# Kernel optimization log

Hardware: AMD Instinct MI355X
Metric: run time of the kernel (lower is better)

Reference implementation:

```python
import jax, jax.numpy as jnp
import numpy as np

EPS = 1e-6  # EPSILON in the original (undefined there; small stabilizer)
MS = 1      # max_shift_size
FEAT = 128  # memory_feature_size


def setup_inputs() -> dict:
    key = jax.random.key(0)
    ks = jax.random.split(key, 17)
    B, V, E, H, N, F = 64, 10000, 256, 512, 8192, FEAT
    G = 4 * H
    s = 0.02  # param init scale
    return {
        'x': jax.random.randint(ks[0], (B,), 0, V),
        'h': jax.random.normal(ks[1], (B, H)) * 0.1,
        'c': jax.random.normal(ks[2], (B, H)) * 0.1,
        'w_read': jax.random.uniform(ks[3], (B, N)),
        'w_write': jax.random.uniform(ks[4], (B, N)),
        'bank': jax.random.normal(ks[5], (B, N, F)),
        'emb': jax.random.normal(ks[6], (V, E)) * s,
        'W_ih': jax.random.normal(ks[7], (G, E)) * s,
        'b_ih': jnp.zeros((G,)),
        'W_hh': jax.random.normal(ks[8], (G, H)) * s,
        'b_hh': jnp.zeros((G,)),
        'W_read': jax.random.normal(ks[9], (134, H)) * s,
        'b_read': jnp.zeros((134,)),
        'W_write': jax.random.normal(ks[10], (390, H)) * s,
        'b_write': jnp.zeros((390,)),
        'W_out': jax.random.normal(ks[11], (V, F)) * s,
        'b_out': jnp.zeros((V,)),
    }


def _lstm_cell(xe, h, c, W_ih, b_ih, W_hh, b_hh):
    g = xe @ W_ih.T + b_ih + h @ W_hh.T + b_hh  # [B, 4H]
    i, f, gg, o = jnp.split(g, 4, axis=1)
    c2 = jax.nn.sigmoid(f) * c + jax.nn.sigmoid(i) * jnp.tanh(gg)
    h2 = jax.nn.sigmoid(o) * jnp.tanh(c2)
    return h2, c2


def _head_move(bank, w_prev, k, b, g, s, r):
    # content addressing: cosine similarity of key vs each memory row
    mE = bank + EPS                       # [B, N, F]
    kE = k[:, None, :] + EPS              # [B, 1, F]
    num = jnp.sum(mE * kE, axis=-1)       # [B, N]
    den = jnp.linalg.norm(mE, axis=-1) * jnp.linalg.norm(kE, axis=-1)
    sim = num / jnp.maximum(den, 1e-8)
    w = jax.nn.softmax(b * sim, axis=1)
    # interpolation (as written in the source: w + (1-g)*w_prev)
    w = w + (1.0 - g) * w_prev
    # circular shift by location addressing (vectorized conv over modulo pad)
    N = w.shape[1]
    idx = (jnp.arange(N)[:, None] + jnp.arange(-MS, MS + 1)[None, :]) % N  # [N, K]
    w = jnp.einsum('bnk,bk->bn', w[:, idx], s)
    # sharpen
    wr = w ** r
    return wr / (jnp.sum(wr, axis=1, keepdims=True) + EPS)


def _interpret_read(h, W, b):
    o = h @ W.T + b
    F = FEAT
    k = o[:, :F]
    beta = jax.nn.softplus(o[:, F:F + 1])
    g = jax.nn.sigmoid(o[:, F + 1:F + 2])
    s = jax.nn.softmax(o[:, F + 2:F + 2 + (2 * MS + 1)], axis=1)
    r = 1.0 + jax.nn.softplus(o[:, F + 2 + (2 * MS + 1):F + 3 + (2 * MS + 1)])
    return k, beta, g, s, r


def _interpret_write(h, W, b):
    o = h @ W.T + b
    F = FEAT
    k, beta, g, s, r = _interpret_read(h, W[:F + 3 + (2 * MS + 1)], b[:F + 3 + (2 * MS + 1)])
    base = F + 3 + (2 * MS + 1)
    e = jax.nn.sigmoid(o[:, base:base + F])
    a = o[:, base + F:base + 2 * F]
    return k, beta, g, s, r, e, a


def reference(x, h, c, w_read, w_write, bank, emb, W_ih, b_ih, W_hh, b_hh,
              W_read, b_read, W_write, b_write, W_out, b_out):
    # controller
    xe = emb[x]                                  # [B, E]
    h2, c2 = _lstm_cell(xe, h, c, W_ih, b_ih, W_hh, b_hh)
    # write head + memory write
    k, beta, g, s, r, e, a = _interpret_write(h2, W_write, b_write)
    ww = _head_move(bank, w_write, k, beta, g, s, r)   # [B, N]
    bank2 = bank * (1.0 - ww[:, :, None] * e[:, None, :]) + ww[:, :, None] * a[:, None, :]
    # read head + memory read (uses updated bank)
    k, beta, g, s, r = _interpret_read(h2, W_read, b_read)
    wr = _head_move(bank2, w_read, k, beta, g, s, r)
    rvec = jnp.sum(wr[:, :, None] * bank2, axis=1)     # [B, F]
    return rvec @ W_out.T + b_out                      # [B, V]
```

## Files before the change

kernel.cpp:

```cpp
#include <hip/hip_runtime.h>
#include <math.h>

#define BB   64
#define NN   8192
#define FF   128
#define HH   512
#define GG   2048
#define EE   256
#define VV   10000
#define EPSF 1e-6f

static constexpr size_t OFF_XT    = 0;
static constexpr size_t OFF_G     = OFF_XT   + 49152;
static constexpr size_t OFF_H2T   = OFF_G    + 131072;
static constexpr size_t OFF_OCAT  = OFF_H2T  + 32768;
static constexpr size_t OFF_PAR   = OFF_OCAT + 33536;
static constexpr size_t OFF_ZW    = OFF_PAR  + 34816;
static constexpr size_t OFF_SR    = OFF_ZW   + 524288;
static constexpr size_t OFF_WW    = OFF_SR   + 4194304;
static constexpr size_t OFF_WR    = OFF_WW   + 524288;
static constexpr size_t OFF_WRWW  = OFF_WR   + 524288;
static constexpr size_t OFF_PT    = OFF_WRWW + 524288;
static constexpr size_t OFF_T3    = OFF_PT   + 524288;
static constexpr size_t OFF_RVEC  = OFF_T3   + 64;

__device__ __forceinline__ float sigmoidf_(float x){ return 1.f/(1.f + __expf(-x)); }
__device__ __forceinline__ float softplusf_(float x){ return (x > 20.f) ? x : log1pf(__expf(x)); }

__global__ __launch_bounds__(256) void gather_xt_kernel(
    const int* __restrict__ x, const float* __restrict__ h,
    const float* __restrict__ emb, float* __restrict__ Xt)
{
  const int idx = blockIdx.x*256 + threadIdx.x;
  const int k = idx >> 6, b = idx & 63;
  float v = (k < EE) ? emb[(size_t)x[b]*EE + k] : h[(size_t)b*HH + (k - EE)];
  Xt[(size_t)k*64 + b] = v;
}

__global__ __launch_bounds__(256) void lstm_gates_kernel(
    const float* __restrict__ Xt, const float* __restrict__ Wih,
    const float* __restrict__ bih, const float* __restrict__ Whh,
    const float* __restrict__ bhh, float* __restrict__ g)
{
  const int tid = threadIdx.x;
  const int wv = __builtin_amdgcn_readfirstlane(tid >> 6);
  const int lane = tid & 63;
  const int j = blockIdx.x*4 + wv;
  const float* wi = Wih + (size_t)j*EE;
  const float* wh = Whh + (size_t)j*HH;
  float acc = bih[j] + bhh[j];
  #pragma unroll 8
  for (int k = 0; k < EE; ++k)
    acc = fmaf(wi[k], Xt[(size_t)k*64 + lane], acc);
  #pragma unroll 8
  for (int k = 0; k < HH; ++k)
    acc = fmaf(wh[k], Xt[(size_t)(EE+k)*64 + lane], acc);
  g[(size_t)j*64 + lane] = acc;
}

__global__ __launch_bounds__(256) void lstm_act_kernel(
    const float* __restrict__ g, const float* __restrict__ c,
    float* __restrict__ h2t)
{
  const int idx = blockIdx.x*256 + threadIdx.x;
  const int bb = idx & 63, hh = idx >> 6;
  const float gi = g[(size_t)(hh)*64 + bb];
  const float gf = g[(size_t)(512+hh)*64 + bb];
  const float gg = g[(size_t)(1024+hh)*64 + bb];
  const float go = g[(size_t)(1536+hh)*64 + bb];
  const float c0 = c[(size_t)bb*HH + hh];
  const float c2 = sigmoidf_(gf)*c0 + sigmoidf_(gi)*tanhf(gg);
  h2t[(size_t)hh*64 + bb] = sigmoidf_(go)*tanhf(c2);
}

__global__ __launch_bounds__(256) void head_gemm_kernel(
    const float* __restrict__ h2t, const float* __restrict__ Ww,
    const float* __restrict__ bw, const float* __restrict__ Wr,
    const float* __restrict__ br, float* __restrict__ ocat)
{
  const int tid = threadIdx.x;
  const int wv = __builtin_amdgcn_readfirstlane(tid >> 6);
  const int lane = tid & 63;
  const int j = blockIdx.x*4 + wv;
  const float* wrow = (j < 390) ? (Ww + (size_t)j*HH) : (Wr + (size_t)(j-390)*HH);
  float acc = (j < 390) ? bw[j] : br[j-390];
  #pragma unroll 8
  for (int k = 0; k < HH; ++k)
    acc = fmaf(wrow[k], h2t[(size_t)k*64 + lane], acc);
  ocat[(size_t)j*64 + lane] = acc;
}

__global__ void interpret_kernel(const float* __restrict__ ocat,
                                 float* __restrict__ params)
{
  const int b = blockIdx.x, l = threadIdx.x;
  float* P = params + (size_t)b*544;
  float skw = 0.f, skr = 0.f, sakr = 0.f, sa2 = 0.f;
  #pragma unroll
  for (int f = l; f < 128; f += 64){
    float kwE = ocat[(size_t)f*64 + b] + EPSF;
    float ee  = sigmoidf_(ocat[(size_t)(134+f)*64 + b]);
    float aa  = ocat[(size_t)(262+f)*64 + b];
    float krE = ocat[(size_t)(390+f)*64 + b] + EPSF;
    P[f] = kwE; P[128+f] = krE; P[256+f] = aa; P[384+f] = ee;
    skw = fmaf(kwE,kwE,skw); skr = fmaf(krE,krE,skr);
    sakr = fmaf(aa,krE,sakr); sa2 = fmaf(aa,aa,sa2);
  }
  #pragma unroll
  for (int m = 32; m >= 1; m >>= 1){
    skw += __shfl_xor(skw,m); skr += __shfl_xor(skr,m);
    sakr += __shfl_xor(sakr,m); sa2 += __shfl_xor(sa2,m);
  }
  if (l == 0){
    P[512+0] = softplusf_(ocat[(size_t)128*64 + b]);
    P[512+1] = sigmoidf_(ocat[(size_t)129*64 + b]);
    {
      float x0 = ocat[(size_t)130*64+b], x1 = ocat[(size_t)131*64+b], x2 = ocat[(size_t)132*64+b];
      float mm = fmaxf(x0, fmaxf(x1, x2));
      float e0 = __expf(x0-mm), e1 = __expf(x1-mm), e2 = __expf(x2-mm);
      float s = e0+e1+e2;
      P[512+2] = e0/s; P[512+3] = e1/s; P[512+4] = e2/s;
    }
    P[512+5] = 1.f + softplusf_(ocat[(size_t)133*64 + b]);
    P[512+6] = softplusf_(ocat[(size_t)518*64 + b]);
    P[512+7] = sigmoidf_(ocat[(size_t)519*64 + b]);
    {
      float x0 = ocat[(size_t)520*64+b], x1 = ocat[(size_t)521*64+b], x2 = ocat[(size_t)522*64+b];
      float mm = fmaxf(x0, fmaxf(x1, x2));
      float e0 = __expf(x0-mm), e1 = __expf(x1-mm), e2 = __expf(x2-mm);
      float s = e0+e1+e2;
      P[512+8] = e0/s; P[512+9] = e1/s; P[512+10] = e2/s;
    }
    P[512+11] = 1.f + softplusf_(ocat[(size_t)523*64 + b]);
    P[512+12] = sqrtf(skw); P[512+13] = sqrtf(skr);
    P[512+14] = sakr;       P[512+15] = sa2;
  }
}

__global__ __launch_bounds__(256) void pass_a_kernel(
    const float* __restrict__ bank, const float* __restrict__ params,
    float* __restrict__ zw, float* __restrict__ Sr)
{
  const int blk = blockIdx.x;
  const int b = blk >> 5, chunk = blk & 31;
  const int tid = threadIdx.x;
  const int wv = tid >> 6, lane = tid & 63;
  const int fslot = lane & 7, rsub = lane >> 3;
  const float* P = params + (size_t)b*544;
  const int fb = fslot << 4;
  float kw[16], kr[16], av[16], ev[16];
  #pragma unroll
  for (int i = 0; i < 16; ++i){
    kw[i] = P[fb+i]; kr[i] = P[128+fb+i]; av[i] = P[256+fb+i]; ev[i] = P[384+fb+i];
  }
  const float beta_w = P[512+0], nkw = P[512+12];
  for (int it = 0; it < 8; ++it){
    const int n = (chunk << 8) + (it << 5) + (wv << 3) + rsub;
    const size_t row = (size_t)b*NN + n;
    const float4* m4 = reinterpret_cast<const float4*>(bank + row*FF + fb);
    float mv[16];
    *reinterpret_cast<float4*>(&mv[0])  = m4[0];
    *reinterpret_cast<float4*>(&mv[4])  = m4[1];
    *reinterpret_cast<float4*>(&mv[8])  = m4[2];
    *reinterpret_cast<float4*>(&mv[12]) = m4[3];
    float s1=0.f,s2=0.f,s3=0.f,s4=0.f,s5=0.f,s6=0.f,s7=0.f,s8=0.f;
    #pragma unroll
    for (int i = 0; i < 16; ++i){
      const float m = mv[i], u = m + EPSF, em = ev[i]*m;
      s1 = fmaf(u,kw[i],s1);  s2 = fmaf(u,u,s2);
      s3 = fmaf(u,kr[i],s3);  s4 = fmaf(em,kr[i],s4);
      s5 = fmaf(u,av[i],s5);  s6 = fmaf(u,em,s6);
      s7 = fmaf(av[i],em,s7); s8 = fmaf(em,em,s8);
    }
    #pragma unroll
    for (int mm = 1; mm < 8; mm <<= 1){
      s1 += __shfl_xor(s1,mm); s2 += __shfl_xor(s2,mm);
      s3 += __shfl_xor(s3,mm); s4 += __shfl_xor(s4,mm);
      s5 += __shfl_xor(s5,mm); s6 += __shfl_xor(s6,mm);
      s7 += __shfl_xor(s7,mm); s8 += __shfl_xor(s8,mm);
    }
    if (fslot == 0){
      float sim = s1 / fmaxf(sqrtf(s2)*nkw, 1e-8f);
      zw[row] = beta_w * sim;
      float4* o = reinterpret_cast<float4*>(Sr + row*8);
      o[0] = make_float4(s2,s3,s4,s5);
      o[1] = make_float4(s6,s7,s8,0.f);
    }
  }
}

__device__ __forceinline__ float blockMax1024(float v, float* red, int tid){
  #pragma unroll
  for (int m = 32; m >= 1; m >>= 1) v = fmaxf(v, __shfl_xor(v,m));
  __syncthreads();
  if ((tid & 63) == 0) red[tid >> 6] = v;
  __syncthreads();
  if (tid == 0){
    float r = red[0];
    #pragma unroll
    for (int i = 1; i < 16; ++i) r = fmaxf(r, red[i]);
    red[16] = r;
  }
  __syncthreads();
  return red[16];
}
__device__ __forceinline__ float blockSum1024(float v, float* red, int tid){
  #pragma unroll
  for (int m = 32; m >= 1; m >>= 1) v += __shfl_xor(v,m);
  __syncthreads();
  if ((tid & 63) == 0) red[tid >> 6] = v;
  __syncthreads();
  if (tid == 0){
    float r = 0.f;
    #pragma unroll
    for (int i = 0; i < 16; ++i) r += red[i];
    red[16] = r;
  }
  __syncthreads();
  return red[16];
}

__global__ __launch_bounds__(1024) void head_pipeline_kernel(
    const float* __restrict__ zw, const float* __restrict__ Sr,
    const float* __restrict__ w_write, const float* __restrict__ w_read,
    const float* __restrict__ params,
    float* __restrict__ wwg, float* __restrict__ wrg,
    float* __restrict__ wrwwg, float* __restrict__ T3g)
{
  __shared__ float wa[NN];
  __shared__ float red[32];
  const int b = blockIdx.x;
  const int tid = threadIdx.x;
  const float* P = params + (size_t)b*544 + 512;
  const float g_w = P[1], sw0 = P[2], sw1 = P[3], sw2 = P[4], r_w = P[5];
  const float beta_r = P[6], g_r = P[7], sr0 = P[8], sr1 = P[9], sr2 = P[10], r_r = P[11];
  const float nkr = P[13], C_akr = P[14], Ca2 = P[15];
  const size_t base = (size_t)b*NN;
  float cv[8], wwreg[8];

  float lm = -1e30f;
  #pragma unroll
  for (int i = 0; i < 8; ++i){ int n = tid + (i<<10); float z = zw[base+n]; wa[n] = z; lm = fmaxf(lm,z); }
  float M = blockMax1024(lm, red, tid);
  float ls = 0.f;
  #pragma unroll
  for (int i = 0; i < 8; ++i){ int n = tid + (i<<10); float e = __expf(wa[n]-M); wa[n] = e; ls += e; }
  float S = blockSum1024(ls, red, tid);
  const float invS = 1.f/S;
  #pragma unroll
  for (int i = 0; i < 8; ++i){ int n = tid + (i<<10); wa[n] = wa[n]*invS + (1.f-g_w)*w_write[base+n]; }
  __syncthreads();
  #pragma unroll
  for (int i = 0; i < 8; ++i){ int n = tid + (i<<10);
    cv[i] = sw0*wa[(n+NN-1)&(NN-1)] + sw1*wa[n] + sw2*wa[(n+1)&(NN-1)]; }
  __syncthreads();
  float lp = 0.f;
  #pragma unroll
  for (int i = 0; i < 8; ++i){ int n = tid + (i<<10); float p = __expf(r_w*__logf(cv[i])); wa[n] = p; lp += p; }
  float Sp = blockSum1024(lp, red, tid);
  float inv = 1.f/(Sp + EPSF);
  #pragma unroll
  for (int i = 0; i < 8; ++i){ int n = tid + (i<<10); float ww = wa[n]*inv; wwreg[i] = ww; wwg[base+n] = ww; }
  __syncthreads();

  lm = -1e30f;
  #pragma unroll
  for (int i = 0; i < 8; ++i){
    int n = tid + (i<<10);
    const size_t row = base + n;
    const float4* s4 = reinterpret_cast<const float4*>(Sr) + row*2;
    float4 A = s4[0], Bv = s4[1];
    float ww = wwreg[i];
    float num = A.y + ww*(C_akr - A.z);
    float d2  = A.x + 2.f*ww*(A.w - Bv.x) + ww*ww*(Ca2 - 2.f*Bv.y + Bv.z);
    float den = sqrtf(d2)*nkr;
    float z = beta_r * (num / fmaxf(den, 1e-8f));
    wa[n] = z; lm = fmaxf(lm,z);
  }
  M = blockMax1024(lm, red, tid);
  ls = 0.f;
  #pragma unroll
  for (int i = 0; i < 8; ++i){ int n = tid + (i<<10); float e = __expf(wa[n]-M); wa[n] = e; ls += e; }
  S = blockSum1024(ls, red, tid);
  const float invS2 = 1.f/S;
  #pragma unroll
  for (int i = 0; i < 8; ++i){ int n = tid + (i<<10); wa[n] = wa[n]*invS2 + (1.f-g_r)*w_read[base+n]; }
  __syncthreads();
  #pragma unroll
  for (int i = 0; i < 8; ++i){ int n = tid + (i<<10);
    cv[i] = sr0*wa[(n+NN-1)&(NN-1)] + sr1*wa[n] + sr2*wa[(n+1)&(NN-1)]; }
  __syncthreads();
  lp = 0.f;
  #pragma unroll
  for (int i = 0; i < 8; ++i){ int n = tid + (i<<10); float p = __expf(r_r*__logf(cv[i])); wa[n] = p; lp += p; }
  Sp = blockSum1024(lp, red, tid);
  inv = 1.f/(Sp + EPSF);
  float t3 = 0.f;
  #pragma unroll
  for (int i = 0; i < 8; ++i){
    int n = tid + (i<<10);
    float wr_ = wa[n]*inv;
    wrg[base+n] = wr_;
    float xx = wr_*wwreg[i];
    wrwwg[base+n] = xx;
    t3 += xx;
  }
  float T3 = blockSum1024(t3, red, tid);
  if (tid == 0) T3g[b] = T3;
}

__global__ __launch_bounds__(256) void pass_d_kernel(
    const float* __restrict__ bank, const float* __restrict__ wrg,
    const float* __restrict__ wrwwg, float* __restrict__ pT)
{
  const int blk = blockIdx.x;
  const int b = blk >> 5, chunk = blk & 31;
  const int tid = threadIdx.x;
  const int st = tid >> 5, li = tid & 31;
  float4 a1 = make_float4(0.f,0.f,0.f,0.f);
  float4 a2 = make_float4(0.f,0.f,0.f,0.f);
  for (int it = 0; it < 32; ++it){
    const int n = (chunk << 8) + (it << 3) + st;
    const size_t row = (size_t)b*NN + n;
    const float w1 = wrg[row], w2 = wrwwg[row];
    const float4 m = reinterpret_cast<const float4*>(bank + row*FF)[li];
    a1.x = fmaf(w1,m.x,a1.x); a1.y = fmaf(w1,m.y,a1.y);
    a1.z = fmaf(w1,m.z,a1.z); a1.w = fmaf(w1,m.w,a1.w);
    a2.x = fmaf(w2,m.x,a2.x); a2.y = fmaf(w2,m.y,a2.y);
    a2.z = fmaf(w2,m.z,a2.z); a2.w = fmaf(w2,m.w,a2.w);
  }
  __shared__ float lds[8*256];
  *reinterpret_cast<float4*>(&lds[st*256 + li*4]) = a1;
  *reinterpret_cast<float4*>(&lds[st*256 + 128 + li*4]) = a2;
  __syncthreads();
  float s = 0.f;
  #pragma unroll
  for (int k = 0; k < 8; ++k) s += lds[k*256 + tid];
  pT[(size_t)blk*256 + tid] = s;
}

__global__ __launch_bounds__(256) void rvec_kernel(
    const float* __restrict__ pT, const float* __restrict__ params,
    const float* __restrict__ T3g, float* __restrict__ rvec)
{
  const int gid = blockIdx.x*256 + threadIdx.x;
  const int b = gid >> 7, f = gid & 127;
  float t1 = 0.f, t2 = 0.f;
  for (int cc = 0; cc < 32; ++cc){
    const float* p = pT + (size_t)((b<<5) + cc)*256;
    t1 += p[f]; t2 += p[128+f];
  }
  const float* P = params + (size_t)b*544;
  rvec[gid] = t1 - P[384+f]*t2 + P[256+f]*T3g[b];
}

__global__ __launch_bounds__(256) void out_gemm_kernel(
    const float* __restrict__ rvec, const float* __restrict__ Wout,
    const float* __restrict__ bout, float* __restrict__ out)
{
  const int tid = threadIdx.x;
  const int wv = __builtin_amdgcn_readfirstlane(tid >> 6);
  const int lane = tid & 63;
  const int j0 = blockIdx.x*32 + wv*8;
  float acc[8];
  #pragma unroll
  for (int jj = 0; jj < 8; ++jj){ int j = j0 + jj; acc[jj] = (j < VV) ? bout[j] : 0.f; }
  for (int fc = 0; fc < 128; fc += 32){
    float rv[32];
    #pragma unroll
    for (int i = 0; i < 32; ++i) rv[i] = rvec[lane*128 + fc + i];
    #pragma unroll
    for (int jj = 0; jj < 8; ++jj){
      const int j = j0 + jj;
      if (j < VV){
        const float* w = Wout + (size_t)j*128 + fc;
        #pragma unroll
        for (int i = 0; i < 32; ++i) acc[jj] = fmaf(w[i], rv[i], acc[jj]);
      }
    }
  }
  #pragma unroll
  for (int jj = 0; jj < 8; ++jj){
    int j = j0 + jj;
    if (j < VV) out[(size_t)lane*VV + j] = acc[jj];
  }
}

extern "C" void kernel_launch(void* const* d_in, const int* in_sizes, int n_in,
                              void* d_out, int out_size, void* d_ws, size_t ws_size,
                              hipStream_t stream)
{
  const int*   x       = (const int*)  d_in[0];
  const float* h       = (const float*)d_in[1];
  const float* c       = (const float*)d_in[2];
  const float* w_read  = (const float*)d_in[3];
  const float* w_write = (const float*)d_in[4];
  const float* bank    = (const float*)d_in[5];
  const float* emb     = (const float*)d_in[6];
  const float* Wih     = (const float*)d_in[7];
  const float* bih     = (const float*)d_in[8];
  const float* Whh     = (const float*)d_in[9];
  const float* bhh     = (const float*)d_in[10];
  const float* Wr      = (const float*)d_in[11];
  const float* br      = (const float*)d_in[12];
  const float* Ww      = (const float*)d_in[13];
  const float* bw      = (const float*)d_in[14];
  const float* Wout    = (const float*)d_in[15];
  const float* bout    = (const float*)d_in[16];
  float* out = (float*)d_out;
  float* ws  = (float*)d_ws;

  float* Xt    = ws + OFF_XT;
  float* gg    = ws + OFF_G;
  float* h2t   = ws + OFF_H2T;
  float* ocat  = ws + OFF_OCAT;
  float* par   = ws + OFF_PAR;
  float* zwp   = ws + OFF_ZW;
  float* Srp   = ws + OFF_SR;
  float* wwp   = ws + OFF_WW;
  float* wrp   = ws + OFF_WR;
  float* wrwwp = ws + OFF_WRWW;
  float* pTp   = ws + OFF_PT;
  float* T3p   = ws + OFF_T3;
  float* rvp   = ws + OFF_RVEC;

  hipLaunchKernelGGL(gather_xt_kernel,     dim3(192),  dim3(256), 0, stream, x, h, emb, Xt);
  hipLaunchKernelGGL(lstm_gates_kernel,    dim3(512),  dim3(256), 0, stream, Xt, Wih, bih, Whh, bhh, gg);
  hipLaunchKernelGGL(lstm_act_kernel,      dim3(128),  dim3(256), 0, stream, gg, c, h2t);
  hipLaunchKernelGGL(head_gemm_kernel,     dim3(131),  dim3(256), 0, stream, h2t, Ww, bw, Wr, br, ocat);
  hipLaunchKernelGGL(interpret_kernel,     dim3(64),   dim3(64),  0, stream, ocat, par);
  hipLaunchKernelGGL(pass_a_kernel,        dim3(2048), dim3(256), 0, stream, bank, par, zwp, Srp);
  hipLaunchKernelGGL(head_pipeline_kernel, dim3(64),   dim3(1024),0, stream, zwp, Srp, w_write, w_read, par, wwp, wrp, wrwwp, T3p);
  hipLaunchKernelGGL(pass_d_kernel,        dim3(2048), dim3(256), 0, stream, bank, wrp, wrwwp, pTp);
  hipLaunchKernelGGL(rvec_kernel,          dim3(32),   dim3(256), 0, stream, pTp, par, T3p, rvp);
  hipLaunchKernelGGL(out_gemm_kernel,      dim3(313),  dim3(256), 0, stream, rvp, Wout, bout, out);
}
```

Baseline: 227.3 us.

## Split-K small GEMMs, compact per-row stats, drop ww store, reverse pass_d order

The LSTM gate and head GEMMs now have each wave compute four output rows over half of K, reusing each loaded input value across rows. Partial sums are written separately and combined, along with biases, in the activation and interpret kernels. pass_a folds the constant terms and now writes 5 floats per row instead of 8, and the unused ww array store is removed, which cuts global traffic in the head pipeline. pass_d walks blocks and rows in reverse order so its first bank reads hit rows pass_a touched last and may still be in cache; the cost is extra partial buffers and more kernels reading them.

Measured after the change: 209.1 us. 1.09x faster.

```diff
diff --git a/kernel.cpp b/kernel.cpp
--- a/kernel.cpp
+++ b/kernel.cpp
@@ -11,18 +11,18 @@
 #define EPSF 1e-6f
 
 static constexpr size_t OFF_XT    = 0;
-static constexpr size_t OFF_G     = OFF_XT   + 49152;
-static constexpr size_t OFF_H2T   = OFF_G    + 131072;
-static constexpr size_t OFF_OCAT  = OFF_H2T  + 32768;
-static constexpr size_t OFF_PAR   = OFF_OCAT + 33536;
-static constexpr size_t OFF_ZW    = OFF_PAR  + 34816;
-static constexpr size_t OFF_SR    = OFF_ZW   + 524288;
-static constexpr size_t OFF_WW    = OFF_SR   + 4194304;
-static constexpr size_t OFF_WR    = OFF_WW   + 524288;
-static constexpr size_t OFF_WRWW  = OFF_WR   + 524288;
-static constexpr size_t OFF_PT    = OFF_WRWW + 524288;
-static constexpr size_t OFF_T3    = OFF_PT   + 524288;
-static constexpr size_t OFF_RVEC  = OFF_T3   + 64;
+static constexpr size_t OFF_GPART = 49152;
+static constexpr size_t OFF_H2T   = 311296;
+static constexpr size_t OFF_HPART = 344064;
+static constexpr size_t OFF_PAR   = 411136;
+static constexpr size_t OFF_ZW    = 445952;
+static constexpr size_t OFF_Q4    = 970240;
+static constexpr size_t OFF_Q1    = 3067392;
+static constexpr size_t OFF_WR    = 3591680;
+static constexpr size_t OFF_WRWW  = 4115968;
+static constexpr size_t OFF_PT    = 4640256;
+static constexpr size_t OFF_T3    = 5164544;
+static constexpr size_t OFF_RVEC  = 5164608;
 
 __device__ __forceinline__ float sigmoidf_(float x){ return 1.f/(1.f + __expf(-x)); }
 __device__ __forceinline__ float softplusf_(float x){ return (x > 20.f) ? x : log1pf(__expf(x)); }
@@ -39,35 +39,64 @@
 
 __global__ __launch_bounds__(256) void lstm_gates_kernel(
     const float* __restrict__ Xt, const float* __restrict__ Wih,
-    const float* __restrict__ bih, const float* __restrict__ Whh,
-    const float* __restrict__ bhh, float* __restrict__ g)
-{
-  const int tid = threadIdx.x;
-  const int wv = __builtin_amdgcn_readfirstlane(tid >> 6);
+    const float* __restrict__ Whh, float* __restrict__ gpart)
+{
+  const int tid = threadIdx.x;
   const int lane = tid & 63;
-  const int j = blockIdx.x*4 + wv;
-  const float* wi = Wih + (size_t)j*EE;
-  const float* wh = Whh + (size_t)j*HH;
-  float acc = bih[j] + bhh[j];
-  #pragma unroll 8
-  for (int k = 0; k < EE; ++k)
-    acc = fmaf(wi[k], Xt[(size_t)k*64 + lane], acc);
-  #pragma unroll 8
-  for (int k = 0; k < HH; ++k)
-    acc = fmaf(wh[k], Xt[(size_t)(EE+k)*64 + lane], acc);
-  g[(size_t)j*64 + lane] = acc;
+  const int gw = __builtin_amdgcn_readfirstlane(blockIdx.x*4 + (tid >> 6));
+  const int jg = gw >> 1, kc = gw & 1;
+  const int j0 = jg << 2;
+  float a0=0.f, a1=0.f, a2=0.f, a3=0.f;
+  if (kc == 0){
+    const float* w0 = Wih + (size_t)(j0+0)*EE;
+    const float* w1 = Wih + (size_t)(j0+1)*EE;
+    const float* w2 = Wih + (size_t)(j0+2)*EE;
+    const float* w3 = Wih + (size_t)(j0+3)*EE;
+    #pragma unroll 4
+    for (int k = 0; k < EE; ++k){
+      const float xv = Xt[(size_t)k*64 + lane];
+      a0 = fmaf(w0[k],xv,a0); a1 = fmaf(w1[k],xv,a1);
+      a2 = fmaf(w2[k],xv,a2); a3 = fmaf(w3[k],xv,a3);
+    }
+    const float* v0 = Whh + (size_t)(j0+0)*HH;
+    const float* v1 = Whh + (size_t)(j0+1)*HH;
+    const float* v2 = Whh + (size_t)(j0+2)*HH;
+    const float* v3 = Whh + (size_t)(j0+3)*HH;
+    #pragma unroll 4
+    for (int k = 0; k < 128; ++k){
+      const float xv = Xt[(size_t)(EE+k)*64 + lane];
+      a0 = fmaf(v0[k],xv,a0); a1 = fmaf(v1[k],xv,a1);
+      a2 = fmaf(v2[k],xv,a2); a3 = fmaf(v3[k],xv,a3);
+    }
+  } else {
+    const float* v0 = Whh + (size_t)(j0+0)*HH;
+    const float* v1 = Whh + (size_t)(j0+1)*HH;
+    const float* v2 = Whh + (size_t)(j0+2)*HH;
+    const float* v3 = Whh + (size_t)(j0+3)*HH;
+    #pragma unroll 4
+    for (int k = 128; k < 512; ++k){
+      const float xv = Xt[(size_t)(EE+k)*64 + lane];
+      a0 = fmaf(v0[k],xv,a0); a1 = fmaf(v1[k],xv,a1);
+      a2 = fmaf(v2[k],xv,a2); a3 = fmaf(v3[k],xv,a3);
+    }
+  }
+  float* gp = gpart + (size_t)kc*131072 + (size_t)j0*64 + lane;
+  gp[0] = a0; gp[64] = a1; gp[128] = a2; gp[192] = a3;
 }
 
 __global__ __launch_bounds__(256) void lstm_act_kernel(
-    const float* __restrict__ g, const float* __restrict__ c,
+    const float* __restrict__ gpart, const float* __restrict__ bih,
+    const float* __restrict__ bhh, const float* __restrict__ c,
     float* __restrict__ h2t)
 {
   const int idx = blockIdx.x*256 + threadIdx.x;
   const int bb = idx & 63, hh = idx >> 6;
-  const float gi = g[(size_t)(hh)*64 + bb];
-  const float gf = g[(size_t)(512+hh)*64 + bb];
-  const float gg = g[(size_t)(1024+hh)*64 + bb];
-  const float go = g[(size_t)(1536+hh)*64 + bb];
+  #define GSUM(j) (gpart[(size_t)(j)*64+bb] + gpart[(size_t)131072+(size_t)(j)*64+bb] + bih[j] + bhh[j])
+  const float gi = GSUM(hh);
+  const float gf = GSUM(512+hh);
+  const float gg = GSUM(1024+hh);
+  const float go = GSUM(1536+hh);
+  #undef GSUM
   const float c0 = c[(size_t)bb*HH + hh];
   const float c2 = sigmoidf_(gf)*c0 + sigmoidf_(gi)*tanhf(gg);
   h2t[(size_t)hh*64 + bb] = sigmoidf_(go)*tanhf(c2);
@@ -75,33 +104,45 @@
 
 __global__ __launch_bounds__(256) void head_gemm_kernel(
     const float* __restrict__ h2t, const float* __restrict__ Ww,
-    const float* __restrict__ bw, const float* __restrict__ Wr,
-    const float* __restrict__ br, float* __restrict__ ocat)
-{
-  const int tid = threadIdx.x;
-  const int wv = __builtin_amdgcn_readfirstlane(tid >> 6);
+    const float* __restrict__ Wr, float* __restrict__ hpart)
+{
+  const int tid = threadIdx.x;
   const int lane = tid & 63;
-  const int j = blockIdx.x*4 + wv;
-  const float* wrow = (j < 390) ? (Ww + (size_t)j*HH) : (Wr + (size_t)(j-390)*HH);
-  float acc = (j < 390) ? bw[j] : br[j-390];
-  #pragma unroll 8
-  for (int k = 0; k < HH; ++k)
-    acc = fmaf(wrow[k], h2t[(size_t)k*64 + lane], acc);
-  ocat[(size_t)j*64 + lane] = acc;
-}
-
-__global__ void interpret_kernel(const float* __restrict__ ocat,
+  const int gw = __builtin_amdgcn_readfirstlane(blockIdx.x*4 + (tid >> 6));
+  const int jg = gw >> 1, kc = gw & 1;
+  if (jg >= 131) return;
+  const int j0 = jg << 2;
+  const float* w0 = (j0+0 < 390) ? (Ww + (size_t)(j0+0)*HH) : (Wr + (size_t)(j0+0-390)*HH);
+  const float* w1 = (j0+1 < 390) ? (Ww + (size_t)(j0+1)*HH) : (Wr + (size_t)(j0+1-390)*HH);
+  const float* w2 = (j0+2 < 390) ? (Ww + (size_t)(j0+2)*HH) : (Wr + (size_t)(j0+2-390)*HH);
+  const float* w3 = (j0+3 < 390) ? (Ww + (size_t)(j0+3)*HH) : (Wr + (size_t)(j0+3-390)*HH);
+  const int k0 = kc << 8;
+  float a0=0.f, a1=0.f, a2=0.f, a3=0.f;
+  #pragma unroll 4
+  for (int k = k0; k < k0+256; ++k){
+    const float xv = h2t[(size_t)k*64 + lane];
+    a0 = fmaf(w0[k],xv,a0); a1 = fmaf(w1[k],xv,a1);
+    a2 = fmaf(w2[k],xv,a2); a3 = fmaf(w3[k],xv,a3);
+  }
+  float* hp = hpart + (size_t)kc*33536 + (size_t)j0*64 + lane;
+  hp[0] = a0; hp[64] = a1; hp[128] = a2; hp[192] = a3;
+}
+
+__global__ void interpret_kernel(const float* __restrict__ hp,
+                                 const float* __restrict__ bw,
+                                 const float* __restrict__ br,
                                  float* __restrict__ params)
 {
   const int b = blockIdx.x, l = threadIdx.x;
   float* P = params + (size_t)b*544;
+  #define OC(j) (hp[(size_t)(j)*64+b] + hp[(size_t)33536+(size_t)(j)*64+b])
   float skw = 0.f, skr = 0.f, sakr = 0.f, sa2 = 0.f;
   #pragma unroll
   for (int f = l; f < 128; f += 64){
-    float kwE = ocat[(size_t)f*64 + b] + EPSF;
-    float ee  = sigmoidf_(ocat[(size_t)(134+f)*64 + b]);
-    float aa  = ocat[(size_t)(262+f)*64 + b];
-    float krE = ocat[(size_t)(390+f)*64 + b] + EPSF;
+    float kwE = OC(f) + bw[f] + EPSF;
+    float ee  = sigmoidf_(OC(134+f) + bw[134+f]);
+    float aa  = OC(262+f) + bw[262+f];
+    float krE = OC(390+f) + br[f] + EPSF;
     P[f] = kwE; P[128+f] = krE; P[256+f] = aa; P[384+f] = ee;
     skw = fmaf(kwE,kwE,skw); skr = fmaf(krE,krE,skr);
     sakr = fmaf(aa,krE,sakr); sa2 = fmaf(aa,aa,sa2);
@@ -112,34 +153,35 @@
     sakr += __shfl_xor(sakr,m); sa2 += __shfl_xor(sa2,m);
   }
   if (l == 0){
-    P[512+0] = softplusf_(ocat[(size_t)128*64 + b]);
-    P[512+1] = sigmoidf_(ocat[(size_t)129*64 + b]);
+    P[512+0] = softplusf_(OC(128) + bw[128]);
+    P[512+1] = sigmoidf_(OC(129) + bw[129]);
     {
-      float x0 = ocat[(size_t)130*64+b], x1 = ocat[(size_t)131*64+b], x2 = ocat[(size_t)132*64+b];
+      float x0 = OC(130)+bw[130], x1 = OC(131)+bw[131], x2 = OC(132)+bw[132];
       float mm = fmaxf(x0, fmaxf(x1, x2));
       float e0 = __expf(x0-mm), e1 = __expf(x1-mm), e2 = __expf(x2-mm);
       float s = e0+e1+e2;
       P[512+2] = e0/s; P[512+3] = e1/s; P[512+4] = e2/s;
     }
-    P[512+5] = 1.f + softplusf_(ocat[(size_t)133*64 + b]);
-    P[512+6] = softplusf_(ocat[(size_t)518*64 + b]);
-    P[512+7] = sigmoidf_(ocat[(size_t)519*64 + b]);
+    P[512+5] = 1.f + softplusf_(OC(133) + bw[133]);
+    P[512+6] = softplusf_(OC(518) + br[128]);
+    P[512+7] = sigmoidf_(OC(519) + br[129]);
     {
-      float x0 = ocat[(size_t)520*64+b], x1 = ocat[(size_t)521*64+b], x2 = ocat[(size_t)522*64+b];
+      float x0 = OC(520)+br[130], x1 = OC(521)+br[131], x2 = OC(522)+br[132];
       float mm = fmaxf(x0, fmaxf(x1, x2));
       float e0 = __expf(x0-mm), e1 = __expf(x1-mm), e2 = __expf(x2-mm);
       float s = e0+e1+e2;
       P[512+8] = e0/s; P[512+9] = e1/s; P[512+10] = e2/s;
     }
-    P[512+11] = 1.f + softplusf_(ocat[(size_t)523*64 + b]);
+    P[512+11] = 1.f + softplusf_(OC(523) + br[133]);
     P[512+12] = sqrtf(skw); P[512+13] = sqrtf(skr);
     P[512+14] = sakr;       P[512+15] = sa2;
   }
+  #undef OC
 }
 
 __global__ __launch_bounds__(256) void pass_a_kernel(
     const float* __restrict__ bank, const float* __restrict__ params,
-    float* __restrict__ zw, float* __restrict__ Sr)
+    float* __restrict__ zw, float4* __restrict__ q4, float* __restrict__ q1)
 {
   const int blk = blockIdx.x;
   const int b = blk >> 5, chunk = blk & 31;
@@ -154,6 +196,7 @@
     kw[i] = P[fb+i]; kr[i] = P[128+fb+i]; av[i] = P[256+fb+i]; ev[i] = P[384+fb+i];
   }
   const float beta_w = P[512+0], nkw = P[512+12];
+  const float C_akr = P[512+14], Ca2 = P[512+15];
   for (int it = 0; it < 8; ++it){
     const int n = (chunk << 8) + (it << 5) + (wv << 3) + rsub;
     const size_t row = (size_t)b*NN + n;
@@ -182,9 +225,8 @@
     if (fslot == 0){
       float sim = s1 / fmaxf(sqrtf(s2)*nkw, 1e-8f);
       zw[row] = beta_w * sim;
-      float4* o = reinterpret_cast<float4*>(Sr + row*8);
-      o[0] = make_float4(s2,s3,s4,s5);
-      o[1] = make_float4(s6,s7,s8,0.f);
+      q4[row] = make_float4(s2, s3, C_akr - s4, s5 - s6);
+      q1[row] = Ca2 - 2.f*s7 + s8;
     }
   }
 }
@@ -221,11 +263,11 @@
 }
 
 __global__ __launch_bounds__(1024) void head_pipeline_kernel(
-    const float* __restrict__ zw, const float* __restrict__ Sr,
+    const float* __restrict__ zw, const float4* __restrict__ q4,
+    const float* __restrict__ q1,
     const float* __restrict__ w_write, const float* __restrict__ w_read,
     const float* __restrict__ params,
-    float* __restrict__ wwg, float* __restrict__ wrg,
-    float* __restrict__ wrwwg, float* __restrict__ T3g)
+    float* __restrict__ wrg, float* __restrict__ wrwwg, float* __restrict__ T3g)
 {
   __shared__ float wa[NN];
   __shared__ float red[32];
@@ -234,7 +276,7 @@
   const float* P = params + (size_t)b*544 + 512;
   const float g_w = P[1], sw0 = P[2], sw1 = P[3], sw2 = P[4], r_w = P[5];
   const float beta_r = P[6], g_r = P[7], sr0 = P[8], sr1 = P[9], sr2 = P[10], r_r = P[11];
-  const float nkr = P[13], C_akr = P[14], Ca2 = P[15];
+  const float nkr = P[13];
   const size_t base = (size_t)b*NN;
   float cv[8], wwreg[8];
 
@@ -260,7 +302,7 @@
   float Sp = blockSum1024(lp, red, tid);
   float inv = 1.f/(Sp + EPSF);
   #pragma unroll
-  for (int i = 0; i < 8; ++i){ int n = tid + (i<<10); float ww = wa[n]*inv; wwreg[i] = ww; wwg[base+n] = ww; }
+  for (int i = 0; i < 8; ++i){ wwreg[i] = wa[tid + (i<<10)]*inv; }
   __syncthreads();
 
   lm = -1e30f;
@@ -268,11 +310,11 @@
   for (int i = 0; i < 8; ++i){
     int n = tid + (i<<10);
     const size_t row = base + n;
-    const float4* s4 = reinterpret_cast<const float4*>(Sr) + row*2;
-    float4 A = s4[0], Bv = s4[1];
+    const float4 q = q4[row];
+    const float qq = q1[row];
     float ww = wwreg[i];
-    float num = A.y + ww*(C_akr - A.z);
-    float d2  = A.x + 2.f*ww*(A.w - Bv.x) + ww*ww*(Ca2 - 2.f*Bv.y + Bv.z);
+    float num = q.y + ww*q.z;
+    float d2  = q.x + 2.f*ww*q.w + ww*ww*qq;
     float den = sqrtf(d2)*nkr;
     float z = beta_r * (num / fmaxf(den, 1e-8f));
     wa[n] = z; lm = fmaxf(lm,z);
@@ -313,13 +355,13 @@
     const float* __restrict__ bank, const float* __restrict__ wrg,
     const float* __restrict__ wrwwg, float* __restrict__ pT)
 {
-  const int blk = blockIdx.x;
+  const int blk = 2047 - blockIdx.x;
   const int b = blk >> 5, chunk = blk & 31;
   const int tid = threadIdx.x;
   const int st = tid >> 5, li = tid & 31;
   float4 a1 = make_float4(0.f,0.f,0.f,0.f);
   float4 a2 = make_float4(0.f,0.f,0.f,0.f);
-  for (int it = 0; it < 32; ++it){
+  for (int it = 31; it >= 0; --it){
     const int n = (chunk << 8) + (it << 3) + st;
     const size_t row = (size_t)b*NN + n;
     const float w1 = wrg[row], w2 = wrwwg[row];
@@ -411,13 +453,13 @@
   float* ws  = (float*)d_ws;
 
   float* Xt    = ws + OFF_XT;
-  float* gg    = ws + OFF_G;
+  float* gpart = ws + OFF_GPART;
   float* h2t   = ws + OFF_H2T;
-  float* ocat  = ws + OFF_OCAT;
+  float* hpart = ws + OFF_HPART;
   float* par   = ws + OFF_PAR;
   float* zwp   = ws + OFF_ZW;
-  float* Srp   = ws + OFF_SR;
-  float* wwp   = ws + OFF_WW;
+  float4* q4p  = reinterpret_cast<float4*>(ws + OFF_Q4);
+  float* q1p   = ws + OFF_Q1;
   float* wrp   = ws + OFF_WR;
   float* wrwwp = ws + OFF_WRWW;
   float* pTp   = ws + OFF_PT;
@@ -425,12 +467,12 @@
   float* rvp   = ws + OFF_RVEC;
 
   hipLaunchKernelGGL(gather_xt_kernel,     dim3(192),  dim3(256), 0, stream, x, h, emb, Xt);
-  hipLaunchKernelGGL(lstm_gates_kernel,    dim3(512),  dim3(256), 0, stream, Xt, Wih, bih, Whh, bhh, gg);
-  hipLaunchKernelGGL(lstm_act_kernel,      dim3(128),  dim3(256), 0, stream, gg, c, h2t);
-  hipLaunchKernelGGL(head_gemm_kernel,     dim3(131),  dim3(256), 0, stream, h2t, Ww, bw, Wr, br, ocat);
-  hipLaunchKernelGGL(interpret_kernel,     dim3(64),   dim3(64),  0, stream, ocat, par);
-  hipLaunchKernelGGL(pass_a_kernel,        dim3(2048), dim3(256), 0, stream, bank, par, zwp, Srp);
-  hipLaunchKernelGGL(head_pipeline_kernel, dim3(64),   dim3(1024),0, stream, zwp, Srp, w_write, w_read, par, wwp, wrp, wrwwp, T3p);
+  hipLaunchKernelGGL(lstm_gates_kernel,    dim3(256),  dim3(256), 0, stream, Xt, Wih, Whh, gpart);
+  hipLaunchKernelGGL(lstm_act_kernel,      dim3(128),  dim3(256), 0, stream, gpart, bih, bhh, c, h2t);
+  hipLaunchKernelGGL(head_gemm_kernel,     dim3(66),   dim3(256), 0, stream, h2t, Ww, Wr, hpart);
+  hipLaunchKernelGGL(interpret_kernel,     dim3(64),   dim3(64),  0, stream, hpart, bw, br, par);
+  hipLaunchKernelGGL(pass_a_kernel,        dim3(2048), dim3(256), 0, stream, bank, par, zwp, q4p, q1p);
+  hipLaunchKernelGGL(head_pipeline_kernel, dim3(64),   dim3(1024),0, stream, zwp, q4p, q1p, w_write, w_read, par, wrp, wrwwp, T3p);
   hipLaunchKernelGGL(pass_d_kernel,        dim3(2048), dim3(256), 0, stream, bank, wrp, wrwwp, pTp);
   hipLaunchKernelGGL(rvec_kernel,          dim3(32),   dim3(256), 0, stream, pTp, par, T3p, rvp);
   hipLaunchKernelGGL(out_gemm_kernel,      dim3(313),  dim3(256), 0, stream, rvp, Wout, bout, out);
```
